# Kernel tuning notes

Hardware: AMD Instinct MI355X
Metric: run time of the kernel (lower is better)

## Reference

```python
import jax, jax.numpy as jnp
import numpy as np
import math

EMBED_DIM = 256
NUM_HEADS = 8
HEAD_DIM = EMBED_DIM // NUM_HEADS
SEQ = 512
BSZ = 2


def setup_inputs() -> dict:
    key = jax.random.key(0)
    ks = jax.random.split(key, 9)
    def xavier(k, shape):
        fan_in, fan_out = shape[1], shape[0]
        bound = math.sqrt(6.0 / (fan_in + fan_out))
        return jax.random.uniform(k, shape, jnp.float32, -bound, bound)
    return {
        "query": jax.random.normal(ks[0], (SEQ, BSZ, EMBED_DIM), jnp.float32),
        "key": jax.random.normal(ks[1], (SEQ, BSZ, EMBED_DIM), jnp.float32),
        "value": jax.random.normal(ks[2], (SEQ, BSZ, EMBED_DIM), jnp.float32),
        "rel_pos_embedding": jax.random.normal(ks[3], (BSZ, SEQ, SEQ, EMBED_DIM), jnp.float32),
        "attn_mask": jax.random.normal(ks[4], (SEQ, SEQ), jnp.float32),
        "in_proj_weight": xavier(ks[5], (3 * EMBED_DIM, EMBED_DIM)),
        "in_proj_bias": jnp.zeros((3 * EMBED_DIM,), jnp.float32),
        "out_proj_weight": xavier(ks[6], (EMBED_DIM, EMBED_DIM)),
        "out_proj_bias": jnp.zeros((EMBED_DIM,), jnp.float32),
    }


def reference(query, key, value, rel_pos_embedding, attn_mask,
              in_proj_weight, in_proj_bias, out_proj_weight, out_proj_bias):
    L, B, E = query.shape
    H, D = NUM_HEADS, HEAD_DIM
    # NOTE: original module projects ONLY the query and chunks into q,k,v
    qkv = query @ in_proj_weight.T + in_proj_bias          # (L,B,3E)
    q, k, v = jnp.split(qkv, 3, axis=-1)                    # each (L,B,E)
    # (L,B,E) -> (B*H, L, D)
    def to_heads(t):
        return jnp.swapaxes(t.reshape(L, B * H, D), 0, 1)
    q, k, v = to_heads(q), to_heads(k), to_heads(v)
    scores = jnp.einsum('nld,nmd->nlm', q, k) / math.sqrt(D)  # (B*H,L,L)
    # relative position bias: einsum over UNSCALED q
    q4 = q.reshape(B, H, L, D)
    rel = rel_pos_embedding.reshape(B, L, L, H, D)
    rel_bias = jnp.einsum('bhld,blmhd->bhlm', q4, rel)        # (B,H,L,L)
    scores = scores.reshape(B, H, L, L) + rel_bias
    # additive 2D attn_mask broadcast over batch and heads
    scores = scores + attn_mask[None, None, :, :]
    scores = scores.reshape(B * H, L, L)
    attn = jax.nn.softmax(scores, axis=-1)                    # (B*H,L,L)
    out = jnp.einsum('nlm,nmd->nld', attn, v)                 # (B*H,L,D)
    out = jnp.swapaxes(out, 0, 1).reshape(L, B, E)            # (L,B,E)
    out = out @ out_proj_weight.T + out_proj_bias
    return out, attn
```

## Files before the change

kernel.cpp:

```cpp
#include <hip/hip_runtime.h>
#include <math.h>

#define L_SEQ 512
#define BSZ 2
#define NH 8
#define HD 32
#define E 256
#define SCALE 0.17677669529663687f

typedef float f32x4 __attribute__((ext_vector_type(4)));


__global__ void inproj_kernel(const float* __restrict__ query,
                              const float* __restrict__ W,
                              const float* __restrict__ bias,
                              float* __restrict__ q2,
                              float* __restrict__ k2,
                              float* __restrict__ vh) {
    int r0 = blockIdx.x * 4;
    int t = threadIdx.x;
    __shared__ float xs[4][E];
#pragma unroll
    for (int r = 0; r < 4; ++r) xs[r][t] = query[(size_t)(r0 + r) * E + t];
    __syncthreads();

    int c  = t & 7;
    int cg = t >> 3;

#pragma unroll
    for (int p = 0; p < 3; ++p) {
#pragma unroll
        for (int pass = 0; pass < 8; ++pass) {
            int col = pass * 32 + cg;
            const float4* wp = (const float4*)(W + (size_t)(p * E + col) * E);
            float a0 = 0.f, a1 = 0.f, a2 = 0.f, a3 = 0.f;
#pragma unroll
            for (int kk = 0; kk < 8; ++kk) {
                float4 w  = wp[c + kk * 8];
                float4 x0 = ((const float4*)xs[0])[c + kk * 8];
                float4 x1 = ((const float4*)xs[1])[c + kk * 8];
                float4 x2 = ((const float4*)xs[2])[c + kk * 8];
                float4 x3 = ((const float4*)xs[3])[c + kk * 8];
                a0 += w.x * x0.x + w.y * x0.y + w.z * x0.z + w.w * x0.w;
                a1 += w.x * x1.x + w.y * x1.y + w.z * x1.z + w.w * x1.w;
                a2 += w.x * x2.x + w.y * x2.y + w.z * x2.z + w.w * x2.w;
                a3 += w.x * x3.x + w.y * x3.y + w.z * x3.z + w.w * x3.w;
            }
#pragma unroll
            for (int off = 1; off <= 4; off <<= 1) {
                a0 += __shfl_xor(a0, off);
                a1 += __shfl_xor(a1, off);
                a2 += __shfl_xor(a2, off);
                a3 += __shfl_xor(a3, off);
            }
            if (c == 0) {
                float bb = bias[p * E + col];
                float res[4] = {a0, a1, a2, a3};
#pragma unroll
                for (int r = 0; r < 4; ++r) {
                    int row = r0 + r, l = row >> 1, b = row & 1;
                    float val = res[r] + bb;
                    if (p == 0) {
                        q2[((size_t)b * L_SEQ + l) * E + col] = val;
                    } else if (p == 1) {
                        k2[((size_t)b * L_SEQ + l) * E + col] = val;
                    } else {
                        int h = col >> 5, d = col & 31;
                        vh[((size_t)(b * NH + h) * L_SEQ + l) * HD + d] = val;
                    }
                }
            }
        }
    }
}

__global__ void attn_kernel(const float* __restrict__ q2,
                            const float* __restrict__ k2,
                            const float* __restrict__ vh,
                            const float* __restrict__ rpe,
                            const float* __restrict__ mask,
                            float* __restrict__ attn_out,
                            float* __restrict__ oh2) {
    int bid = blockIdx.x;
    int b = bid >> 9, l = bid & (L_SEQ - 1);
    int t = threadIdx.x;
    int lane = t & 63, wid = t >> 6;

    __shared__ float qs[E];
    __shared__ float s_lds[NH][L_SEQ + 1];

    if (t < E) qs[t] = q2[((size_t)b * L_SEQ + l) * E + t];
    __syncthreads();

    float4 qc = ((const float4*)qs)[lane];
    int h1 = lane >> 3;
    const float* kbase = k2 + (size_t)b * L_SEQ * E;
    const float* rbase = rpe + ((size_t)(b * L_SEQ + l)) * L_SEQ * E;

#pragma unroll 4
    for (int i = 0; i < 64; ++i) {
        int m = wid * 64 + i;
        float4 kv = ((const float4*)(kbase + (size_t)m * E))[lane];
        f32x4 rv = __builtin_nontemporal_load(((const f32x4*)(rbase + (size_t)m * E)) + lane);
        float part = (kv.x * qc.x + kv.y * qc.y + kv.z * qc.z + kv.w * qc.w) * SCALE
                   +  rv.x * qc.x + rv.y * qc.y + rv.z * qc.z + rv.w * qc.w;
        part += __shfl_xor(part, 1);
        part += __shfl_xor(part, 2);
        part += __shfl_xor(part, 4);
        if ((lane & 7) == 0) s_lds[h1][m] = part;
    }
    __syncthreads();

    int h = wid;
    const float* mrow = mask + (size_t)l * L_SEQ;
    float sv[8];
    float mx = -1e30f;
#pragma unroll
    for (int i = 0; i < 8; ++i) {
        int m = i * 64 + lane;
        sv[i] = s_lds[h][m] + mrow[m];
        mx = fmaxf(mx, sv[i]);
    }
#pragma unroll
    for (int off = 32; off > 0; off >>= 1) mx = fmaxf(mx, __shfl_xor(mx, off));
    float sum = 0.f;
#pragma unroll
    for (int i = 0; i < 8; ++i) { sv[i] = __expf(sv[i] - mx); sum += sv[i]; }
#pragma unroll
    for (int off = 32; off > 0; off >>= 1) sum += __shfl_xor(sum, off);
    float inv = 1.0f / sum;

    float* arow = attn_out + ((size_t)(b * NH + h) * L_SEQ + l) * L_SEQ;
#pragma unroll
    for (int i = 0; i < 8; ++i) {
        int m = i * 64 + lane;
        float pn = sv[i] * inv;
        arow[m] = pn;
        s_lds[h][m] = pn;
    }

    int dq = lane & 7, mg = lane >> 3;
    const float4* vbase = (const float4*)(vh + (size_t)(b * NH + h) * L_SEQ * HD);
    float4 acc = {0.f, 0.f, 0.f, 0.f};
#pragma unroll 4
    for (int i = 0; i < 64; ++i) {
        int m = i * 8 + mg;
        float4 v4 = vbase[(size_t)m * 8 + dq];
        float p = s_lds[h][m];
        acc.x += p * v4.x; acc.y += p * v4.y; acc.z += p * v4.z; acc.w += p * v4.w;
    }
#pragma unroll
    for (int off = 8; off <= 32; off <<= 1) {
        acc.x += __shfl_xor(acc.x, off);
        acc.y += __shfl_xor(acc.y, off);
        acc.z += __shfl_xor(acc.z, off);
        acc.w += __shfl_xor(acc.w, off);
    }
    if (mg == 0) {
        ((float4*)(oh2 + ((size_t)b * L_SEQ + l) * E))[h * 8 + dq] = acc;
    }
}

__global__ void outproj_kernel(const float* __restrict__ oh2,
                               const float* __restrict__ W,
                               const float* __restrict__ bias,
                               float* __restrict__ out) {
    int r0 = blockIdx.x * 4;
    int t = threadIdx.x;
    __shared__ float xs[4][E];
#pragma unroll
    for (int r = 0; r < 4; ++r) {
        int row = r0 + r, l = row >> 1, b = row & 1;
        xs[r][t] = oh2[((size_t)b * L_SEQ + l) * E + t];
    }
    __syncthreads();

    int c  = t & 7;
    int cg = t >> 3;
#pragma unroll
    for (int pass = 0; pass < 8; ++pass) {
        int col = pass * 32 + cg;
        const float4* wp = (const float4*)(W + (size_t)col * E);
        float a0 = 0.f, a1 = 0.f, a2 = 0.f, a3 = 0.f;
#pragma unroll
        for (int kk = 0; kk < 8; ++kk) {
            float4 w  = wp[c + kk * 8];
            float4 x0 = ((const float4*)xs[0])[c + kk * 8];
            float4 x1 = ((const float4*)xs[1])[c + kk * 8];
            float4 x2 = ((const float4*)xs[2])[c + kk * 8];
            float4 x3 = ((const float4*)xs[3])[c + kk * 8];
            a0 += w.x * x0.x + w.y * x0.y + w.z * x0.z + w.w * x0.w;
            a1 += w.x * x1.x + w.y * x1.y + w.z * x1.z + w.w * x1.w;
            a2 += w.x * x2.x + w.y * x2.y + w.z * x2.z + w.w * x2.w;
            a3 += w.x * x3.x + w.y * x3.y + w.z * x3.z + w.w * x3.w;
        }
#pragma unroll
        for (int off = 1; off <= 4; off <<= 1) {
            a0 += __shfl_xor(a0, off);
            a1 += __shfl_xor(a1, off);
            a2 += __shfl_xor(a2, off);
            a3 += __shfl_xor(a3, off);
        }
        if (c == 0) {
            float bb = bias[col];
            float res[4] = {a0, a1, a2, a3};
#pragma unroll
            for (int r = 0; r < 4; ++r) {
                out[(size_t)(r0 + r) * E + col] = res[r] + bb;
            }
        }
    }
}

extern "C" void kernel_launch(void* const* d_in, const int* in_sizes, int n_in,
                              void* d_out, int out_size, void* d_ws, size_t ws_size,
                              hipStream_t stream) {
    const float* query = (const float*)d_in[0];
    const float* rpe   = (const float*)d_in[3];
    const float* mask  = (const float*)d_in[4];
    const float* Win   = (const float*)d_in[5];
    const float* bin   = (const float*)d_in[6];
    const float* Wout  = (const float*)d_in[7];
    const float* bout  = (const float*)d_in[8];

    float* out  = (float*)d_out;
    float* attn = (float*)d_out + (size_t)L_SEQ * BSZ * E;

    float* q2  = (float*)d_ws;
    float* k2  = q2 + (size_t)BSZ * L_SEQ * E;
    float* vh  = k2 + (size_t)BSZ * L_SEQ * E;
    float* oh2 = vh + (size_t)BSZ * NH * L_SEQ * HD;

    inproj_kernel<<<(L_SEQ * BSZ) / 4, E, 0, stream>>>(query, Win, bin, q2, k2, vh);
    attn_kernel<<<BSZ * L_SEQ, 512, 0, stream>>>(q2, k2, vh, rpe, mask, attn, oh2);
    outproj_kernel<<<(L_SEQ * BSZ) / 4, E, 0, stream>>>(oh2, Wout, bout, out);
}
```

Measured before the change: 165.1 us.

## Split QK scores into separate kernel, use DPP reductions, widen projection grids

Moves the scaled q·k dot products and mask addition out of the rel-pos streaming loop into a new qk_kernel that keeps per-head K tiles in registers and writes a full scores buffer. The attention kernel then only streams the large rel_pos_embedding, reducing each octet with DPP adds instead of shuffles, and reads the precomputed scores. The in/out projection kernels split their columns across a second grid dimension for more parallelism and fuse the q/k/v weight loops. The trade-off is an extra 8M-float scores buffer written and read back through global memory, plus one more kernel launch.

Result: slower. 188.5 us (+14.2%).

```diff
diff --git a/kernel.cpp b/kernel.cpp
--- a/kernel.cpp
+++ b/kernel.cpp
@@ -7,66 +7,82 @@
 #define HD 32
 #define E 256
 #define SCALE 0.17677669529663687f
+#define SROW 520
 
 typedef float f32x4 __attribute__((ext_vector_type(4)));
+
+template <int CTRL>
+__device__ __forceinline__ float dpp_add(float x) {
+    return x + __int_as_float(
+        __builtin_amdgcn_update_dpp(0, __float_as_int(x), CTRL, 0xF, 0xF, true));
+}
+__device__ __forceinline__ float octet_allsum(float x) {
+    x = dpp_add<0xB1>(x);
+    x = dpp_add<0x4E>(x);
+    x = dpp_add<0x141>(x);
+    return x;
+}
 
 
 __global__ void inproj_kernel(const float* __restrict__ query,
                               const float* __restrict__ W,
                               const float* __restrict__ bias,
                               float* __restrict__ q2,
-                              float* __restrict__ k2,
+                              float* __restrict__ kh,
                               float* __restrict__ vh) {
     int r0 = blockIdx.x * 4;
+    int y  = blockIdx.y;
     int t = threadIdx.x;
     __shared__ float xs[4][E];
 #pragma unroll
     for (int r = 0; r < 4; ++r) xs[r][t] = query[(size_t)(r0 + r) * E + t];
     __syncthreads();
 
-    int c  = t & 7;
-    int cg = t >> 3;
-
-#pragma unroll
-    for (int p = 0; p < 3; ++p) {
-#pragma unroll
-        for (int pass = 0; pass < 8; ++pass) {
-            int col = pass * 32 + cg;
-            const float4* wp = (const float4*)(W + (size_t)(p * E + col) * E);
-            float a0 = 0.f, a1 = 0.f, a2 = 0.f, a3 = 0.f;
-#pragma unroll
-            for (int kk = 0; kk < 8; ++kk) {
-                float4 w  = wp[c + kk * 8];
-                float4 x0 = ((const float4*)xs[0])[c + kk * 8];
-                float4 x1 = ((const float4*)xs[1])[c + kk * 8];
-                float4 x2 = ((const float4*)xs[2])[c + kk * 8];
-                float4 x3 = ((const float4*)xs[3])[c + kk * 8];
-                a0 += w.x * x0.x + w.y * x0.y + w.z * x0.z + w.w * x0.w;
-                a1 += w.x * x1.x + w.y * x1.y + w.z * x1.z + w.w * x1.w;
-                a2 += w.x * x2.x + w.y * x2.y + w.z * x2.z + w.w * x2.w;
-                a3 += w.x * x3.x + w.y * x3.y + w.z * x3.z + w.w * x3.w;
+    int c = t & 7, cg = t >> 3;
+#pragma unroll
+    for (int pp = 0; pp < 4; ++pp) {
+        int pass = y * 4 + pp;
+        int col = pass * 32 + cg;
+        float a[3][4];
+#pragma unroll
+        for (int p = 0; p < 3; ++p)
+#pragma unroll
+            for (int r = 0; r < 4; ++r) a[p][r] = 0.f;
+
+#pragma unroll
+        for (int kk = 0; kk < 8; ++kk) {
+            float4 x0 = ((const float4*)xs[0])[c + kk * 8];
+            float4 x1 = ((const float4*)xs[1])[c + kk * 8];
+            float4 x2 = ((const float4*)xs[2])[c + kk * 8];
+            float4 x3 = ((const float4*)xs[3])[c + kk * 8];
+#pragma unroll
+            for (int p = 0; p < 3; ++p) {
+                float4 w = ((const float4*)(W + (size_t)(p * E + col) * E))[c + kk * 8];
+                a[p][0] += w.x * x0.x + w.y * x0.y + w.z * x0.z + w.w * x0.w;
+                a[p][1] += w.x * x1.x + w.y * x1.y + w.z * x1.z + w.w * x1.w;
+                a[p][2] += w.x * x2.x + w.y * x2.y + w.z * x2.z + w.w * x2.w;
+                a[p][3] += w.x * x3.x + w.y * x3.y + w.z * x3.z + w.w * x3.w;
             }
-#pragma unroll
-            for (int off = 1; off <= 4; off <<= 1) {
-                a0 += __shfl_xor(a0, off);
-                a1 += __shfl_xor(a1, off);
-                a2 += __shfl_xor(a2, off);
-                a3 += __shfl_xor(a3, off);
-            }
-            if (c == 0) {
+        }
+#pragma unroll
+        for (int p = 0; p < 3; ++p)
+#pragma unroll
+            for (int r = 0; r < 4; ++r) a[p][r] = octet_allsum(a[p][r]);
+
+        if (c == 0) {
+#pragma unroll
+            for (int p = 0; p < 3; ++p) {
                 float bb = bias[p * E + col];
-                float res[4] = {a0, a1, a2, a3};
 #pragma unroll
                 for (int r = 0; r < 4; ++r) {
                     int row = r0 + r, l = row >> 1, b = row & 1;
-                    float val = res[r] + bb;
+                    float val = a[p][r] + bb;
                     if (p == 0) {
                         q2[((size_t)b * L_SEQ + l) * E + col] = val;
-                    } else if (p == 1) {
-                        k2[((size_t)b * L_SEQ + l) * E + col] = val;
                     } else {
                         int h = col >> 5, d = col & 31;
-                        vh[((size_t)(b * NH + h) * L_SEQ + l) * HD + d] = val;
+                        float* dst = (p == 1) ? kh : vh;
+                        dst[((size_t)(b * NH + h) * L_SEQ + l) * HD + d] = val;
                     }
                 }
             }
@@ -74,11 +90,52 @@
     }
 }
 
+__global__ void qk_kernel(const float* __restrict__ q2,
+                          const float* __restrict__ kh,
+                          const float* __restrict__ mask,
+                          float* __restrict__ scores) {
+    int n = blockIdx.x;
+    int b = n >> 3, h = n & 7;
+    int l0 = blockIdx.y * 32;
+    int t = threadIdx.x, lane = t & 63, w = t >> 6;
+
+    __shared__ float qs[32][32];
+    {
+        int row = t >> 3, quad = t & 7;
+        float4 qv = *(const float4*)(q2 + ((size_t)b * L_SEQ + l0 + row) * E + h * HD + quad * 4);
+        ((float4*)qs[row])[quad] = qv;
+    }
+    __syncthreads();
+
+    f32x4 ka[8], kb[8];
+    const float* kbase = kh + (size_t)n * L_SEQ * HD;
+    {
+        const f32x4* pa = (const f32x4*)(kbase + (size_t)(w * 128 + lane) * HD);
+        const f32x4* pb = (const f32x4*)(kbase + (size_t)(w * 128 + 64 + lane) * HD);
+#pragma unroll
+        for (int i = 0; i < 8; ++i) { ka[i] = pa[i]; kb[i] = pb[i]; }
+    }
+
+    for (int li = 0; li < 32; ++li) {
+        int l = l0 + li;
+        float da = 0.f, db = 0.f;
+#pragma unroll
+        for (int i = 0; i < 8; ++i) {
+            float4 qv = ((const float4*)qs[li])[i];
+            da += ka[i].x * qv.x + ka[i].y * qv.y + ka[i].z * qv.z + ka[i].w * qv.w;
+            db += kb[i].x * qv.x + kb[i].y * qv.y + kb[i].z * qv.z + kb[i].w * qv.w;
+        }
+        size_t off = ((size_t)n * L_SEQ + l) * L_SEQ;
+        const float* mrow = mask + (size_t)l * L_SEQ;
+        scores[off + w * 128 + lane]      = da * SCALE + mrow[w * 128 + lane];
+        scores[off + w * 128 + 64 + lane] = db * SCALE + mrow[w * 128 + 64 + lane];
+    }
+}
+
 __global__ void attn_kernel(const float* __restrict__ q2,
-                            const float* __restrict__ k2,
                             const float* __restrict__ vh,
                             const float* __restrict__ rpe,
-                            const float* __restrict__ mask,
+                            const float* __restrict__ scores,
                             float* __restrict__ attn_out,
                             float* __restrict__ oh2) {
     int bid = blockIdx.x;
@@ -87,38 +144,37 @@
     int lane = t & 63, wid = t >> 6;
 
     __shared__ float qs[E];
-    __shared__ float s_lds[NH][L_SEQ + 1];
+    __shared__ float s_lds[NH * SROW];
 
     if (t < E) qs[t] = q2[((size_t)b * L_SEQ + l) * E + t];
     __syncthreads();
 
-    float4 qc = ((const float4*)qs)[lane];
-    int h1 = lane >> 3;
-    const float* kbase = k2 + (size_t)b * L_SEQ * E;
+    f32x4 qc = ((const f32x4*)qs)[lane];
+    int csel = lane & 7, h1 = lane >> 3;
     const float* rbase = rpe + ((size_t)(b * L_SEQ + l)) * L_SEQ * E;
 
-#pragma unroll 4
-    for (int i = 0; i < 64; ++i) {
-        int m = wid * 64 + i;
-        float4 kv = ((const float4*)(kbase + (size_t)m * E))[lane];
-        f32x4 rv = __builtin_nontemporal_load(((const f32x4*)(rbase + (size_t)m * E)) + lane);
-        float part = (kv.x * qc.x + kv.y * qc.y + kv.z * qc.z + kv.w * qc.w) * SCALE
-                   +  rv.x * qc.x + rv.y * qc.y + rv.z * qc.z + rv.w * qc.w;
-        part += __shfl_xor(part, 1);
-        part += __shfl_xor(part, 2);
-        part += __shfl_xor(part, 4);
-        if ((lane & 7) == 0) s_lds[h1][m] = part;
+    for (int ii = 0; ii < 8; ++ii) {
+        float keep = 0.f;
+#pragma unroll
+        for (int i8 = 0; i8 < 8; ++i8) {
+            int m = wid * 64 + ii * 8 + i8;
+            f32x4 rv = __builtin_nontemporal_load(((const f32x4*)(rbase + (size_t)m * E)) + lane);
+            float part = rv.x * qc.x + rv.y * qc.y + rv.z * qc.z + rv.w * qc.w;
+            part = octet_allsum(part);
+            keep = (i8 == csel) ? part : keep;
+        }
+        s_lds[h1 * SROW + wid * 64 + ii * 8 + csel] = keep;
     }
     __syncthreads();
 
     int h = wid;
-    const float* mrow = mask + (size_t)l * L_SEQ;
+    const float* srow = scores + ((size_t)(b * NH + h) * L_SEQ + l) * L_SEQ;
     float sv[8];
     float mx = -1e30f;
 #pragma unroll
     for (int i = 0; i < 8; ++i) {
         int m = i * 64 + lane;
-        sv[i] = s_lds[h][m] + mrow[m];
+        sv[i] = s_lds[h * SROW + m] + srow[m];
         mx = fmaxf(mx, sv[i]);
     }
 #pragma unroll
@@ -136,17 +192,17 @@
         int m = i * 64 + lane;
         float pn = sv[i] * inv;
         arow[m] = pn;
-        s_lds[h][m] = pn;
+        s_lds[h * SROW + m] = pn;
     }
 
     int dq = lane & 7, mg = lane >> 3;
-    const float4* vbase = (const float4*)(vh + (size_t)(b * NH + h) * L_SEQ * HD);
+    const f32x4* vbase = (const f32x4*)(vh + (size_t)(b * NH + h) * L_SEQ * HD);
     float4 acc = {0.f, 0.f, 0.f, 0.f};
 #pragma unroll 4
     for (int i = 0; i < 64; ++i) {
         int m = i * 8 + mg;
-        float4 v4 = vbase[(size_t)m * 8 + dq];
-        float p = s_lds[h][m];
+        f32x4 v4 = vbase[(size_t)m * 8 + dq];
+        float p = s_lds[h * SROW + m];
         acc.x += p * v4.x; acc.y += p * v4.y; acc.z += p * v4.z; acc.w += p * v4.w;
     }
 #pragma unroll
@@ -166,6 +222,7 @@
                                const float* __restrict__ bias,
                                float* __restrict__ out) {
     int r0 = blockIdx.x * 4;
+    int y  = blockIdx.y;
     int t = threadIdx.x;
     __shared__ float xs[4][E];
 #pragma unroll
@@ -175,10 +232,10 @@
     }
     __syncthreads();
 
-    int c  = t & 7;
-    int cg = t >> 3;
-#pragma unroll
-    for (int pass = 0; pass < 8; ++pass) {
+    int c = t & 7, cg = t >> 3;
+#pragma unroll
+    for (int pp = 0; pp < 4; ++pp) {
+        int pass = y * 4 + pp;
         int col = pass * 32 + cg;
         const float4* wp = (const float4*)(W + (size_t)col * E);
         float a0 = 0.f, a1 = 0.f, a2 = 0.f, a3 = 0.f;
@@ -194,13 +251,8 @@
             a2 += w.x * x2.x + w.y * x2.y + w.z * x2.z + w.w * x2.w;
             a3 += w.x * x3.x + w.y * x3.y + w.z * x3.z + w.w * x3.w;
         }
-#pragma unroll
-        for (int off = 1; off <= 4; off <<= 1) {
-            a0 += __shfl_xor(a0, off);
-            a1 += __shfl_xor(a1, off);
-            a2 += __shfl_xor(a2, off);
-            a3 += __shfl_xor(a3, off);
-        }
+        a0 = octet_allsum(a0); a1 = octet_allsum(a1);
+        a2 = octet_allsum(a2); a3 = octet_allsum(a3);
         if (c == 0) {
             float bb = bias[col];
             float res[4] = {a0, a1, a2, a3};
@@ -226,12 +278,14 @@
     float* out  = (float*)d_out;
     float* attn = (float*)d_out + (size_t)L_SEQ * BSZ * E;
 
-    float* q2  = (float*)d_ws;
-    float* k2  = q2 + (size_t)BSZ * L_SEQ * E;
-    float* vh  = k2 + (size_t)BSZ * L_SEQ * E;
-    float* oh2 = vh + (size_t)BSZ * NH * L_SEQ * HD;
-
-    inproj_kernel<<<(L_SEQ * BSZ) / 4, E, 0, stream>>>(query, Win, bin, q2, k2, vh);
-    attn_kernel<<<BSZ * L_SEQ, 512, 0, stream>>>(q2, k2, vh, rpe, mask, attn, oh2);
-    outproj_kernel<<<(L_SEQ * BSZ) / 4, E, 0, stream>>>(oh2, Wout, bout, out);
-}
+    float* q2     = (float*)d_ws;
+    float* kh     = q2  + (size_t)BSZ * L_SEQ * E;
+    float* vh     = kh  + (size_t)BSZ * NH * L_SEQ * HD;
+    float* oh2    = vh  + (size_t)BSZ * NH * L_SEQ * HD;
+    float* scores = oh2 + (size_t)BSZ * L_SEQ * E;
+
+    inproj_kernel<<<dim3((L_SEQ * BSZ) / 4, 2), E, 0, stream>>>(query, Win, bin, q2, kh, vh);
+    qk_kernel<<<dim3(BSZ * NH, L_SEQ / 32), 256, 0, stream>>>(q2, kh, mask, scores);
+    attn_kernel<<<BSZ * L_SEQ, 512, 0, stream>>>(q2, vh, rpe, scores, attn, oh2);
+    outproj_kernel<<<dim3((L_SEQ * BSZ) / 4, 2), E, 0, stream>>>(oh2, Wout, bout, out);
+}
```

## Fuse three stages into one cooperative kernel with grid syncs and two-row attention blocks

Applied to the files above, without the earlier changes.

Replaces the three separate launches with a single cooperative kernel that runs the input projection, the attention stage and the output projection as phases separated by grid.sync, falling back to three kernels if occupancy is too low. K is now stored head-major so the score loop reads contiguous per-head K. Each attention block handles two query rows, sharing K and V loads between them. The projections compute 8 rows per block. The rel_pos_embedding stream (about 1 GB) still dominates traffic, so launch savings are small, and per-call occupancy queries plus grid syncs add host and device overhead. Plain loads replace the nontemporal rpe loads.

New measurement: 421.8 us. 155% more time.

```diff
diff --git a/kernel.cpp b/kernel.cpp
--- a/kernel.cpp
+++ b/kernel.cpp
@@ -1,5 +1,8 @@
 #include <hip/hip_runtime.h>
+#include <hip/hip_cooperative_groups.h>
 #include <math.h>
+
+namespace cg = cooperative_groups;
 
 #define L_SEQ 512
 #define BSZ 2
@@ -7,209 +10,258 @@
 #define HD 32
 #define E 256
 #define SCALE 0.17677669529663687f
+#define SROW 520
+#define SL_HALF (NH * SROW)
+#define POOL_FLOATS (2 * E + 2 * SL_HALF)
 
 typedef float f32x4 __attribute__((ext_vector_type(4)));
 
-
-__global__ void inproj_kernel(const float* __restrict__ query,
-                              const float* __restrict__ W,
-                              const float* __restrict__ bias,
-                              float* __restrict__ q2,
-                              float* __restrict__ k2,
-                              float* __restrict__ vh) {
-    int r0 = blockIdx.x * 4;
-    int t = threadIdx.x;
-    __shared__ float xs[4][E];
-#pragma unroll
-    for (int r = 0; r < 4; ++r) xs[r][t] = query[(size_t)(r0 + r) * E + t];
-    __syncthreads();
-
-    int c  = t & 7;
-    int cg = t >> 3;
-
-#pragma unroll
-    for (int p = 0; p < 3; ++p) {
-#pragma unroll
-        for (int pass = 0; pass < 8; ++pass) {
-            int col = pass * 32 + cg;
-            const float4* wp = (const float4*)(W + (size_t)(p * E + col) * E);
-            float a0 = 0.f, a1 = 0.f, a2 = 0.f, a3 = 0.f;
-#pragma unroll
-            for (int kk = 0; kk < 8; ++kk) {
-                float4 w  = wp[c + kk * 8];
-                float4 x0 = ((const float4*)xs[0])[c + kk * 8];
-                float4 x1 = ((const float4*)xs[1])[c + kk * 8];
-                float4 x2 = ((const float4*)xs[2])[c + kk * 8];
-                float4 x3 = ((const float4*)xs[3])[c + kk * 8];
-                a0 += w.x * x0.x + w.y * x0.y + w.z * x0.z + w.w * x0.w;
-                a1 += w.x * x1.x + w.y * x1.y + w.z * x1.z + w.w * x1.w;
-                a2 += w.x * x2.x + w.y * x2.y + w.z * x2.z + w.w * x2.w;
-                a3 += w.x * x3.x + w.y * x3.y + w.z * x3.z + w.w * x3.w;
+__device__ __forceinline__ void phaseA_unit(int u, int t, float (*xs)[E],
+    const float* __restrict__ query, const float* __restrict__ Win,
+    const float* __restrict__ bin,
+    float* __restrict__ q2, float* __restrict__ kh, float* __restrict__ vh)
+{
+    int rg = u >> 2, cgrp = u & 3;
+#pragma unroll
+    for (int j = 0; j < 4; ++j) {
+        int idx = j * 512 + t;
+        int r = idx >> 8, cc = idx & 255;
+        xs[r][cc] = query[(size_t)(rg * 8 + r) * E + cc];
+    }
+    __syncthreads();
+    int c = t & 7, cg2 = t >> 3;
+#pragma unroll
+    for (int pp = 0; pp < 3; ++pp) {
+        int col768 = cgrp * 192 + pp * 64 + cg2;
+        const f32x4* wp = (const f32x4*)(Win + (size_t)col768 * E);
+        float a[8];
+#pragma unroll
+        for (int r = 0; r < 8; ++r) a[r] = 0.f;
+#pragma unroll
+        for (int kk = 0; kk < 8; ++kk) {
+            f32x4 w = wp[c + kk * 8];
+#pragma unroll
+            for (int r = 0; r < 8; ++r) {
+                f32x4 x = ((const f32x4*)xs[r])[c + kk * 8];
+                a[r] += w.x * x.x + w.y * x.y + w.z * x.z + w.w * x.w;
             }
-#pragma unroll
-            for (int off = 1; off <= 4; off <<= 1) {
-                a0 += __shfl_xor(a0, off);
-                a1 += __shfl_xor(a1, off);
-                a2 += __shfl_xor(a2, off);
-                a3 += __shfl_xor(a3, off);
-            }
-            if (c == 0) {
-                float bb = bias[p * E + col];
-                float res[4] = {a0, a1, a2, a3};
-#pragma unroll
-                for (int r = 0; r < 4; ++r) {
-                    int row = r0 + r, l = row >> 1, b = row & 1;
-                    float val = res[r] + bb;
-                    if (p == 0) {
-                        q2[((size_t)b * L_SEQ + l) * E + col] = val;
-                    } else if (p == 1) {
-                        k2[((size_t)b * L_SEQ + l) * E + col] = val;
-                    } else {
-                        int h = col >> 5, d = col & 31;
-                        vh[((size_t)(b * NH + h) * L_SEQ + l) * HD + d] = val;
-                    }
+        }
+#pragma unroll
+        for (int r = 0; r < 8; ++r) {
+            a[r] += __shfl_xor(a[r], 1);
+            a[r] += __shfl_xor(a[r], 2);
+            a[r] += __shfl_xor(a[r], 4);
+        }
+        if (c == 0) {
+            int p = col768 >> 8, col = col768 & 255;
+            float bb = bin[col768];
+#pragma unroll
+            for (int r = 0; r < 8; ++r) {
+                int row = rg * 8 + r, l = row >> 1, b = row & 1;
+                float val = a[r] + bb;
+                if (p == 0) {
+                    q2[((size_t)b * L_SEQ + l) * E + col] = val;
+                } else {
+                    int h = col >> 5, d = col & 31;
+                    float* dst = (p == 1) ? kh : vh;
+                    dst[((size_t)(b * NH + h) * L_SEQ + l) * HD + d] = val;
                 }
             }
         }
     }
-}
-
-__global__ void attn_kernel(const float* __restrict__ q2,
-                            const float* __restrict__ k2,
-                            const float* __restrict__ vh,
-                            const float* __restrict__ rpe,
-                            const float* __restrict__ mask,
-                            float* __restrict__ attn_out,
-                            float* __restrict__ oh2) {
-    int bid = blockIdx.x;
-    int b = bid >> 9, l = bid & (L_SEQ - 1);
-    int t = threadIdx.x;
+    __syncthreads();
+}
+
+__device__ __forceinline__ void phaseB_unit(int u, int t, float* pool,
+    const float* __restrict__ q2, const float* __restrict__ kh,
+    const float* __restrict__ vh, const float* __restrict__ rpe,
+    const float* __restrict__ mask,
+    float* __restrict__ attn_out, float* __restrict__ oh2)
+{
+    float* qs   = pool;
+    float* slds = pool + 2 * E;
     int lane = t & 63, wid = t >> 6;
-
-    __shared__ float qs[E];
-    __shared__ float s_lds[NH][L_SEQ + 1];
-
-    if (t < E) qs[t] = q2[((size_t)b * L_SEQ + l) * E + t];
-    __syncthreads();
-
-    float4 qc = ((const float4*)qs)[lane];
-    int h1 = lane >> 3;
-    const float* kbase = k2 + (size_t)b * L_SEQ * E;
-    const float* rbase = rpe + ((size_t)(b * L_SEQ + l)) * L_SEQ * E;
+    int b = u >> 8, lp = u & 255, l0 = lp * 2;
+
+    {
+        int lsel = t >> 8, cc = t & 255;
+        qs[lsel * E + cc] = q2[((size_t)b * L_SEQ + l0 + lsel) * E + cc];
+    }
+    __syncthreads();
+
+    int cq = lane & 7, h1 = lane >> 3;
+    f32x4 qcA = ((const f32x4*)qs)[lane];
+    f32x4 qcB = ((const f32x4*)(qs + E))[lane];
+    const f32x4* rp = (const f32x4*)(rpe + ((size_t)(b * L_SEQ + l0)) * L_SEQ * E);
+    const float* kb_ = kh + (size_t)(b * NH + h1) * L_SEQ * HD;
 
 #pragma unroll 4
-    for (int i = 0; i < 64; ++i) {
-        int m = wid * 64 + i;
-        float4 kv = ((const float4*)(kbase + (size_t)m * E))[lane];
-        f32x4 rv = __builtin_nontemporal_load(((const f32x4*)(rbase + (size_t)m * E)) + lane);
-        float part = (kv.x * qc.x + kv.y * qc.y + kv.z * qc.z + kv.w * qc.w) * SCALE
-                   +  rv.x * qc.x + rv.y * qc.y + rv.z * qc.z + rv.w * qc.w;
+    for (int i = 0; i < 128; ++i) {
+        int r = i * 8 + wid;
+        int m = r & (L_SEQ - 1);
+        f32x4 rv = rp[(size_t)r * 64 + lane];
+        f32x4 kv = *(const f32x4*)(kb_ + (size_t)m * HD + cq * 4);
+        f32x4 qc = (r & L_SEQ) ? qcB : qcA;
+        float part = rv.x * qc.x + rv.y * qc.y + rv.z * qc.z + rv.w * qc.w
+                   + SCALE * (kv.x * qc.x + kv.y * qc.y + kv.z * qc.z + kv.w * qc.w);
         part += __shfl_xor(part, 1);
         part += __shfl_xor(part, 2);
         part += __shfl_xor(part, 4);
-        if ((lane & 7) == 0) s_lds[h1][m] = part;
+        if (cq == 0) slds[(r >> 9) * SL_HALF + h1 * SROW + m] = part;
     }
     __syncthreads();
 
     int h = wid;
-    const float* mrow = mask + (size_t)l * L_SEQ;
-    float sv[8];
-    float mx = -1e30f;
-#pragma unroll
-    for (int i = 0; i < 8; ++i) {
-        int m = i * 64 + lane;
-        sv[i] = s_lds[h][m] + mrow[m];
-        mx = fmaxf(mx, sv[i]);
-    }
-#pragma unroll
-    for (int off = 32; off > 0; off >>= 1) mx = fmaxf(mx, __shfl_xor(mx, off));
-    float sum = 0.f;
-#pragma unroll
-    for (int i = 0; i < 8; ++i) { sv[i] = __expf(sv[i] - mx); sum += sv[i]; }
-#pragma unroll
-    for (int off = 32; off > 0; off >>= 1) sum += __shfl_xor(sum, off);
-    float inv = 1.0f / sum;
-
-    float* arow = attn_out + ((size_t)(b * NH + h) * L_SEQ + l) * L_SEQ;
-#pragma unroll
-    for (int i = 0; i < 8; ++i) {
-        int m = i * 64 + lane;
-        float pn = sv[i] * inv;
-        arow[m] = pn;
-        s_lds[h][m] = pn;
+#pragma unroll
+    for (int lsel = 0; lsel < 2; ++lsel) {
+        int l = l0 + lsel;
+        const float* mrow = mask + (size_t)l * L_SEQ;
+        float sv[8];
+        float mx = -1e30f;
+#pragma unroll
+        for (int i = 0; i < 8; ++i) {
+            int m = i * 64 + lane;
+            sv[i] = slds[lsel * SL_HALF + h * SROW + m] + mrow[m];
+            mx = fmaxf(mx, sv[i]);
+        }
+#pragma unroll
+        for (int off = 32; off > 0; off >>= 1) mx = fmaxf(mx, __shfl_xor(mx, off));
+        float sum = 0.f;
+#pragma unroll
+        for (int i = 0; i < 8; ++i) { sv[i] = __expf(sv[i] - mx); sum += sv[i]; }
+#pragma unroll
+        for (int off = 32; off > 0; off >>= 1) sum += __shfl_xor(sum, off);
+        float inv = 1.0f / sum;
+        float* arow = attn_out + ((size_t)(b * NH + h) * L_SEQ + l) * L_SEQ;
+#pragma unroll
+        for (int i = 0; i < 8; ++i) {
+            int m = i * 64 + lane;
+            float pn = sv[i] * inv;
+            arow[m] = pn;
+            slds[lsel * SL_HALF + h * SROW + m] = pn;
+        }
     }
 
     int dq = lane & 7, mg = lane >> 3;
-    const float4* vbase = (const float4*)(vh + (size_t)(b * NH + h) * L_SEQ * HD);
-    float4 acc = {0.f, 0.f, 0.f, 0.f};
-#pragma unroll 4
+    const f32x4* vbase = (const f32x4*)(vh + (size_t)(b * NH + h) * L_SEQ * HD);
+    float ax0 = 0, ay0 = 0, az0 = 0, aw0 = 0;
+    float ax1 = 0, ay1 = 0, az1 = 0, aw1 = 0;
+#pragma unroll 8
     for (int i = 0; i < 64; ++i) {
         int m = i * 8 + mg;
-        float4 v4 = vbase[(size_t)m * 8 + dq];
-        float p = s_lds[h][m];
-        acc.x += p * v4.x; acc.y += p * v4.y; acc.z += p * v4.z; acc.w += p * v4.w;
+        f32x4 v4 = vbase[(size_t)m * 8 + dq];
+        float p0 = slds[0 * SL_HALF + h * SROW + m];
+        float p1 = slds[1 * SL_HALF + h * SROW + m];
+        ax0 += p0 * v4.x; ay0 += p0 * v4.y; az0 += p0 * v4.z; aw0 += p0 * v4.w;
+        ax1 += p1 * v4.x; ay1 += p1 * v4.y; az1 += p1 * v4.z; aw1 += p1 * v4.w;
     }
 #pragma unroll
     for (int off = 8; off <= 32; off <<= 1) {
-        acc.x += __shfl_xor(acc.x, off);
-        acc.y += __shfl_xor(acc.y, off);
-        acc.z += __shfl_xor(acc.z, off);
-        acc.w += __shfl_xor(acc.w, off);
+        ax0 += __shfl_xor(ax0, off); ay0 += __shfl_xor(ay0, off);
+        az0 += __shfl_xor(az0, off); aw0 += __shfl_xor(aw0, off);
+        ax1 += __shfl_xor(ax1, off); ay1 += __shfl_xor(ay1, off);
+        az1 += __shfl_xor(az1, off); aw1 += __shfl_xor(aw1, off);
     }
     if (mg == 0) {
-        ((float4*)(oh2 + ((size_t)b * L_SEQ + l) * E))[h * 8 + dq] = acc;
-    }
-}
-
-__global__ void outproj_kernel(const float* __restrict__ oh2,
-                               const float* __restrict__ W,
-                               const float* __restrict__ bias,
-                               float* __restrict__ out) {
-    int r0 = blockIdx.x * 4;
-    int t = threadIdx.x;
-    __shared__ float xs[4][E];
-#pragma unroll
-    for (int r = 0; r < 4; ++r) {
-        int row = r0 + r, l = row >> 1, b = row & 1;
-        xs[r][t] = oh2[((size_t)b * L_SEQ + l) * E + t];
-    }
-    __syncthreads();
-
-    int c  = t & 7;
-    int cg = t >> 3;
-#pragma unroll
-    for (int pass = 0; pass < 8; ++pass) {
-        int col = pass * 32 + cg;
-        const float4* wp = (const float4*)(W + (size_t)col * E);
-        float a0 = 0.f, a1 = 0.f, a2 = 0.f, a3 = 0.f;
-#pragma unroll
-        for (int kk = 0; kk < 8; ++kk) {
-            float4 w  = wp[c + kk * 8];
-            float4 x0 = ((const float4*)xs[0])[c + kk * 8];
-            float4 x1 = ((const float4*)xs[1])[c + kk * 8];
-            float4 x2 = ((const float4*)xs[2])[c + kk * 8];
-            float4 x3 = ((const float4*)xs[3])[c + kk * 8];
-            a0 += w.x * x0.x + w.y * x0.y + w.z * x0.z + w.w * x0.w;
-            a1 += w.x * x1.x + w.y * x1.y + w.z * x1.z + w.w * x1.w;
-            a2 += w.x * x2.x + w.y * x2.y + w.z * x2.z + w.w * x2.w;
-            a3 += w.x * x3.x + w.y * x3.y + w.z * x3.z + w.w * x3.w;
-        }
-#pragma unroll
-        for (int off = 1; off <= 4; off <<= 1) {
-            a0 += __shfl_xor(a0, off);
-            a1 += __shfl_xor(a1, off);
-            a2 += __shfl_xor(a2, off);
-            a3 += __shfl_xor(a3, off);
-        }
-        if (c == 0) {
-            float bb = bias[col];
-            float res[4] = {a0, a1, a2, a3};
-#pragma unroll
-            for (int r = 0; r < 4; ++r) {
-                out[(size_t)(r0 + r) * E + col] = res[r] + bb;
-            }
-        }
-    }
+        float4 o0 = {ax0, ay0, az0, aw0};
+        float4 o1 = {ax1, ay1, az1, aw1};
+        ((float4*)(oh2 + ((size_t)b * L_SEQ + l0) * E))[h * 8 + dq] = o0;
+        ((float4*)(oh2 + ((size_t)b * L_SEQ + l0 + 1) * E))[h * 8 + dq] = o1;
+    }
+    __syncthreads();
+}
+
+__device__ __forceinline__ void phaseC_unit(int u, int t, float (*xs)[E],
+    const float* __restrict__ oh2, const float* __restrict__ Wout,
+    const float* __restrict__ bout, float* __restrict__ out)
+{
+    int rg = u >> 2, cgrp = u & 3;
+#pragma unroll
+    for (int j = 0; j < 4; ++j) {
+        int idx = j * 512 + t;
+        int r = idx >> 8, cc = idx & 255;
+        int row = rg * 8 + r, l = row >> 1, b = row & 1;
+        xs[r][cc] = oh2[((size_t)b * L_SEQ + l) * E + cc];
+    }
+    __syncthreads();
+    int c = t & 7, cg2 = t >> 3;
+    int col = cgrp * 64 + cg2;
+    const f32x4* wp = (const f32x4*)(Wout + (size_t)col * E);
+    float a[8];
+#pragma unroll
+    for (int r = 0; r < 8; ++r) a[r] = 0.f;
+#pragma unroll
+    for (int kk = 0; kk < 8; ++kk) {
+        f32x4 w = wp[c + kk * 8];
+#pragma unroll
+        for (int r = 0; r < 8; ++r) {
+            f32x4 x = ((const f32x4*)xs[r])[c + kk * 8];
+            a[r] += w.x * x.x + w.y * x.y + w.z * x.z + w.w * x.w;
+        }
+    }
+#pragma unroll
+    for (int r = 0; r < 8; ++r) {
+        a[r] += __shfl_xor(a[r], 1);
+        a[r] += __shfl_xor(a[r], 2);
+        a[r] += __shfl_xor(a[r], 4);
+    }
+    if (c == 0) {
+        float bb = bout[col];
+#pragma unroll
+        for (int r = 0; r < 8; ++r) {
+            out[(size_t)(rg * 8 + r) * E + col] = a[r] + bb;
+        }
+    }
+    __syncthreads();
+}
+
+__global__ __launch_bounds__(512, 4)
+void fused_coop(const float* __restrict__ query, const float* __restrict__ rpe,
+                const float* __restrict__ mask, const float* __restrict__ Win,
+                const float* __restrict__ bin, const float* __restrict__ Wout,
+                const float* __restrict__ bout,
+                float* __restrict__ q2, float* __restrict__ kh,
+                float* __restrict__ vh, float* __restrict__ oh2,
+                float* __restrict__ out, float* __restrict__ attn_out)
+{
+    cg::grid_group grid = cg::this_grid();
+    __shared__ __align__(16) float pool[POOL_FLOATS];
+    int t = threadIdx.x, nb = gridDim.x;
+    for (int u = blockIdx.x; u < 512; u += nb)
+        phaseA_unit(u, t, (float(*)[E])pool, query, Win, bin, q2, kh, vh);
+    grid.sync();
+    for (int u = blockIdx.x; u < 512; u += nb)
+        phaseB_unit(u, t, pool, q2, kh, vh, rpe, mask, attn_out, oh2);
+    grid.sync();
+    for (int u = blockIdx.x; u < 512; u += nb)
+        phaseC_unit(u, t, (float(*)[E])pool, oh2, Wout, bout, out);
+}
+
+__global__ __launch_bounds__(512, 4)
+void kA(const float* __restrict__ query, const float* __restrict__ Win,
+        const float* __restrict__ bin, float* __restrict__ q2,
+        float* __restrict__ kh, float* __restrict__ vh)
+{
+    __shared__ __align__(16) float xs[8][E];
+    phaseA_unit(blockIdx.x, threadIdx.x, xs, query, Win, bin, q2, kh, vh);
+}
+
+__global__ __launch_bounds__(512, 4)
+void kB(const float* __restrict__ q2, const float* __restrict__ kh,
+        const float* __restrict__ vh, const float* __restrict__ rpe,
+        const float* __restrict__ mask, float* __restrict__ attn_out,
+        float* __restrict__ oh2)
+{
+    __shared__ __align__(16) float pool[POOL_FLOATS];
+    phaseB_unit(blockIdx.x, threadIdx.x, pool, q2, kh, vh, rpe, mask, attn_out, oh2);
+}
+
+__global__ __launch_bounds__(512, 4)
+void kC(const float* __restrict__ oh2, const float* __restrict__ Wout,
+        const float* __restrict__ bout, float* __restrict__ out)
+{
+    __shared__ __align__(16) float xs[8][E];
+    phaseC_unit(blockIdx.x, threadIdx.x, xs, oh2, Wout, bout, out);
 }
 
 extern "C" void kernel_launch(void* const* d_in, const int* in_sizes, int n_in,
@@ -223,15 +275,34 @@
     const float* Wout  = (const float*)d_in[7];
     const float* bout  = (const float*)d_in[8];
 
-    float* out  = (float*)d_out;
+    float* outp = (float*)d_out;
     float* attn = (float*)d_out + (size_t)L_SEQ * BSZ * E;
 
     float* q2  = (float*)d_ws;
-    float* k2  = q2 + (size_t)BSZ * L_SEQ * E;
-    float* vh  = k2 + (size_t)BSZ * L_SEQ * E;
+    float* kh  = q2 + (size_t)BSZ * L_SEQ * E;
+    float* vh  = kh + (size_t)BSZ * NH * L_SEQ * HD;
     float* oh2 = vh + (size_t)BSZ * NH * L_SEQ * HD;
 
-    inproj_kernel<<<(L_SEQ * BSZ) / 4, E, 0, stream>>>(query, Win, bin, q2, k2, vh);
-    attn_kernel<<<BSZ * L_SEQ, 512, 0, stream>>>(q2, k2, vh, rpe, mask, attn, oh2);
-    outproj_kernel<<<(L_SEQ * BSZ) / 4, E, 0, stream>>>(oh2, Wout, bout, out);
-}
+    int maxB = 0;
+    hipError_t eq = hipOccupancyMaxActiveBlocksPerMultiprocessor(
+        &maxB, (const void*)fused_coop, 512, 0);
+    int dev = 0;
+    hipGetDevice(&dev);
+    int numCU = 0;
+    hipDeviceGetAttribute(&numCU, hipDeviceAttributeMultiprocessorCount, dev);
+    long cap = (long)maxB * (long)numCU;
+
+    if (eq == hipSuccess && cap >= 64) {
+        int gridn = (int)(cap < 512 ? cap : 512);
+        void* args[] = {(void*)&query, (void*)&rpe, (void*)&mask,
+                        (void*)&Win, (void*)&bin, (void*)&Wout, (void*)&bout,
+                        (void*)&q2, (void*)&kh, (void*)&vh, (void*)&oh2,
+                        (void*)&outp, (void*)&attn};
+        hipLaunchCooperativeKernel((void*)fused_coop, dim3(gridn), dim3(512),
+                                   args, 0, stream);
+    } else {
+        kA<<<512, 512, 0, stream>>>(query, Win, bin, q2, kh, vh);
+        kB<<<512, 512, 0, stream>>>(q2, kh, vh, rpe, mask, attn, oh2);
+        kC<<<512, 512, 0, stream>>>(oh2, Wout, bout, outp);
+    }
+}
```
